# Kernel optimization log

Measured on AMD Instinct MI355X. Metric: run time of the kernel, lower is better.

## Reference

```python
import jax, jax.numpy as jnp
import numpy as np

B, N, F, H = 8, 2048, 64, 1

def setup_inputs() -> dict:
    key = jax.random.key(0)
    k1, k2, k3, k4 = jax.random.split(key, 4)
    return {
        "encode": jax.random.normal(k1, (B, N, F), dtype=jnp.float32),
        "kernel": jax.random.normal(k2, (F, H, F), dtype=jnp.float32) * 0.1,
        "attn_kernel_self": jax.random.normal(k3, (F, H, 1), dtype=jnp.float32) * 0.1,
        "attn_kernel_neighs": jax.random.normal(k4, (F, H, 1), dtype=jnp.float32) * 0.1,
    }

def reference(encode, kernel, attn_kernel_self, attn_kernel_neighs):
    # project: [B,N,F] x [F,H,F] -> [B,N,H,F]
    h = jnp.einsum('bni,iho->bnho', encode, kernel)
    # per-node scalar scores: [B,N,H,1]
    a_self = jnp.einsum('bnhi,iho->bnho', h, attn_kernel_self)
    a_neigh = jnp.einsum('bnhi,iho->bnho', h, attn_kernel_neighs)
    # transpose last three axes (...ABC -> ...CBA): [B,1,H,N]
    a_neigh_t = jnp.transpose(a_neigh, (0, 3, 2, 1))
    # broadcast-sum -> [B,N,H,N] dense logits, leaky_relu(alpha=0.2), softmax over neighbors
    logits = jax.nn.leaky_relu(a_self + a_neigh_t, negative_slope=0.2)
    coef = jax.nn.softmax(logits, axis=-1)
    # mean over heads (axis=2) -> [B,N,N]
    return jnp.mean(coef, axis=2)
```

## Files before the change

kernel.cpp:

```cpp
#include <hip/hip_runtime.h>

#define BB 8
#define NN 2048
#define FF 64
#define LOG2E 1.4426950408889634f

typedef float f32x4 __attribute__((ext_vector_type(4)));

__global__ __launch_bounds__(256) void scores_fused(const float* __restrict__ enc,
                                                    const float* __restrict__ kmat,
                                                    const float* __restrict__ aks,
                                                    const float* __restrict__ akn,
                                                    float* __restrict__ S,
                                                    float* __restrict__ T) {
    __shared__ float ws[FF], wn[FF];
    const int tid = threadIdx.x;
    if (tid < FF) {
        float s = 0.f, t = 0.f;
        #pragma unroll
        for (int o = 0; o < FF; ++o) {
            float k = kmat[tid * FF + o];
            s += k * aks[o];
            t += k * akn[o];
        }
        ws[tid] = s;
        wn[tid] = t;
    }
    __syncthreads();

    const int g = blockIdx.x * 256 + tid;
    const f32x4* e4 = (const f32x4*)(enc + (size_t)g * FF);
    const f32x4* w4 = (const f32x4*)ws;
    const f32x4* v4 = (const f32x4*)wn;
    float s = 0.f, t = 0.f;
    #pragma unroll
    for (int j = 0; j < FF / 4; ++j) {
        f32x4 e = e4[j];
        f32x4 w = w4[j];
        f32x4 v = v4[j];
        s += e.x * w.x + e.y * w.y + e.z * w.z + e.w * w.w;
        t += e.x * v.x + e.y * v.y + e.z * v.z + e.w * v.w;
    }
    S[g] = s * LOG2E;
    T[g] = t * LOG2E;
}

__device__ __forceinline__ float waveMax(float v) {
    #pragma unroll
    for (int o = 32; o > 0; o >>= 1) v = fmaxf(v, __shfl_xor(v, o, 64));
    return v;
}
__device__ __forceinline__ float waveSum(float v) {
    #pragma unroll
    for (int o = 32; o > 0; o >>= 1) v += __shfl_xor(v, o, 64);
    return v;
}
__device__ __forceinline__ float lk(float x) { return fmaxf(x, 0.2f * x); }

#define ROWS_PER_WAVE 4

__global__ __launch_bounds__(256) void softmax_kernel(const float* __restrict__ S,
                                                      const float* __restrict__ T,
                                                      float* __restrict__ out) {
    const int wave = threadIdx.x >> 6;
    const int lane = threadIdx.x & 63;
    const int row0 = (blockIdx.x * 4 + wave) * ROWS_PER_WAVE;
    const int b    = row0 >> 11;

    const f32x4* t4 = (const f32x4*)(T + (size_t)b * NN);

    f32x4 t[8];
    float tm = -3.4e38f;
    #pragma unroll
    for (int j = 0; j < 8; ++j) {
        t[j] = t4[lane + 64 * j];
        tm = fmaxf(tm, fmaxf(fmaxf(t[j].x, t[j].y), fmaxf(t[j].z, t[j].w)));
    }
    const float tmax = waveMax(tm);

    #pragma unroll
    for (int r = 0; r < ROWS_PER_WAVE; ++r) {
        const int row = row0 + r;
        const float s = S[row];
        const float M = lk(s + tmax);

        f32x4 e[8];
        float ls = 0.f;
        #pragma unroll
        for (int j = 0; j < 8; ++j) {
            e[j].x = __builtin_exp2f(lk(s + t[j].x) - M);
            e[j].y = __builtin_exp2f(lk(s + t[j].y) - M);
            e[j].z = __builtin_exp2f(lk(s + t[j].z) - M);
            e[j].w = __builtin_exp2f(lk(s + t[j].w) - M);
            ls += (e[j].x + e[j].y) + (e[j].z + e[j].w);
        }
        ls = waveSum(ls);
        const float inv = 1.f / ls;

        f32x4* o4 = (f32x4*)(out + (size_t)row * NN);
        #pragma unroll
        for (int j = 0; j < 8; ++j) {
            f32x4 o;
            o.x = e[j].x * inv; o.y = e[j].y * inv;
            o.z = e[j].z * inv; o.w = e[j].w * inv;
            __builtin_nontemporal_store(o, &o4[lane + 64 * j]);
        }
    }
}

extern "C" void kernel_launch(void* const* d_in, const int* in_sizes, int n_in,
                              void* d_out, int out_size, void* d_ws, size_t ws_size,
                              hipStream_t stream) {
    const float* enc  = (const float*)d_in[0];
    const float* kmat = (const float*)d_in[1];
    const float* aks  = (const float*)d_in[2];
    const float* akn  = (const float*)d_in[3];
    float* out = (float*)d_out;

    float* W = (float*)d_ws;
    float* S = W;
    float* T = W + BB * NN;

    scores_fused<<<BB * NN / 256, 256, 0, stream>>>(enc, kmat, aks, akn, S, T);
    softmax_kernel<<<BB * NN / (4 * ROWS_PER_WAVE), 256, 0, stream>>>(S, T, out);
}
```

Before: 34.16 us.

## Factor leaky-relu softmax exponentials into per-column tables shared in LDS

Because exp2 is monotonic and leaky_relu(x) = max(x, 0.2x), each output element becomes max(A*E[j], B*F[j]). Here E and F are per-column exponentials of the T scores, computed once per block into shared memory, and A and B are per-row scalars. This replaces the per-element exp2 in the hot loop with two multiplies and a max, and batches the four row-sum reductions. It also swaps the nontemporal stores for plain stores and uses a fast reciprocal. The risks are some precision difference from the factored exponentials and extra LDS traffic, in a kernel that is likely bound by output-write bandwidth anyway.

```diff
diff --git a/kernel.cpp b/kernel.cpp
--- a/kernel.cpp
+++ b/kernel.cpp
@@ -4,8 +4,22 @@
 #define NN 2048
 #define FF 64
 #define LOG2E 1.4426950408889634f
+#define ROWS_PER_BLOCK 16
 
 typedef float f32x4 __attribute__((ext_vector_type(4)));
+
+__device__ __forceinline__ float waveMax(float v) {
+    #pragma unroll
+    for (int o = 32; o > 0; o >>= 1) v = fmaxf(v, __shfl_xor(v, o, 64));
+    return v;
+}
+__device__ __forceinline__ float lk(float x) { return fmaxf(x, 0.2f * x); }
+__device__ __forceinline__ f32x4 vmax4(f32x4 a, f32x4 b) {
+    f32x4 r;
+    r.x = fmaxf(a.x, b.x); r.y = fmaxf(a.y, b.y);
+    r.z = fmaxf(a.z, b.z); r.w = fmaxf(a.w, b.w);
+    return r;
+}
 
 __global__ __launch_bounds__(256) void scores_fused(const float* __restrict__ enc,
                                                     const float* __restrict__ kmat,
@@ -45,65 +59,88 @@
     T[g] = t * LOG2E;
 }
 
-__device__ __forceinline__ float waveMax(float v) {
-    #pragma unroll
-    for (int o = 32; o > 0; o >>= 1) v = fmaxf(v, __shfl_xor(v, o, 64));
-    return v;
-}
-__device__ __forceinline__ float waveSum(float v) {
-    #pragma unroll
-    for (int o = 32; o > 0; o >>= 1) v += __shfl_xor(v, o, 64);
-    return v;
-}
-__device__ __forceinline__ float lk(float x) { return fmaxf(x, 0.2f * x); }
-
-#define ROWS_PER_WAVE 4
-
 __global__ __launch_bounds__(256) void softmax_kernel(const float* __restrict__ S,
                                                       const float* __restrict__ T,
                                                       float* __restrict__ out) {
-    const int wave = threadIdx.x >> 6;
-    const int lane = threadIdx.x & 63;
-    const int row0 = (blockIdx.x * 4 + wave) * ROWS_PER_WAVE;
+    __shared__ float Ez[NN];
+    __shared__ float Fz[NN];
+    __shared__ float wred[4];
+
+    const int tid  = threadIdx.x;
+    const int wave = tid >> 6, lane = tid & 63;
+    const int row0 = blockIdx.x * ROWS_PER_BLOCK;
     const int b    = row0 >> 11;
 
     const f32x4* t4 = (const f32x4*)(T + (size_t)b * NN);
+    f32x4 ta = t4[tid];
+    f32x4 tb = t4[tid + 256];
+    float tm = fmaxf(fmaxf(fmaxf(ta.x, ta.y), fmaxf(ta.z, ta.w)),
+                     fmaxf(fmaxf(tb.x, tb.y), fmaxf(tb.z, tb.w)));
+    tm = waveMax(tm);
+    if (lane == 0) wred[wave] = tm;
+    __syncthreads();
+    const float tmax = fmaxf(fmaxf(wred[0], wred[1]), fmaxf(wred[2], wred[3]));
 
-    f32x4 t[8];
-    float tm = -3.4e38f;
+    f32x4* EL = (f32x4*)Ez;
+    f32x4* FL = (f32x4*)Fz;
+    {
+        f32x4 d, E, F;
+        d.x = ta.x - tmax; d.y = ta.y - tmax; d.z = ta.z - tmax; d.w = ta.w - tmax;
+        E.x = __builtin_exp2f(d.x); E.y = __builtin_exp2f(d.y);
+        E.z = __builtin_exp2f(d.z); E.w = __builtin_exp2f(d.w);
+        F.x = __builtin_exp2f(0.2f * d.x); F.y = __builtin_exp2f(0.2f * d.y);
+        F.z = __builtin_exp2f(0.2f * d.z); F.w = __builtin_exp2f(0.2f * d.w);
+        EL[tid] = E; FL[tid] = F;
+        d.x = tb.x - tmax; d.y = tb.y - tmax; d.z = tb.z - tmax; d.w = tb.w - tmax;
+        E.x = __builtin_exp2f(d.x); E.y = __builtin_exp2f(d.y);
+        E.z = __builtin_exp2f(d.z); E.w = __builtin_exp2f(d.w);
+        F.x = __builtin_exp2f(0.2f * d.x); F.y = __builtin_exp2f(0.2f * d.y);
+        F.z = __builtin_exp2f(0.2f * d.z); F.w = __builtin_exp2f(0.2f * d.w);
+        EL[tid + 256] = E; FL[tid + 256] = F;
+    }
+    __syncthreads();
+
+    const int wrow0 = row0 + wave * 4;
+    float A[4], Bc[4], ls[4];
     #pragma unroll
-    for (int j = 0; j < 8; ++j) {
-        t[j] = t4[lane + 64 * j];
-        tm = fmaxf(tm, fmaxf(fmaxf(t[j].x, t[j].y), fmaxf(t[j].z, t[j].w)));
+    for (int r = 0; r < 4; ++r) {
+        const float s = S[wrow0 + r];
+        const float u = s + tmax;
+        const float M = lk(u);
+        A[r]  = __builtin_exp2f(u - M);
+        Bc[r] = __builtin_exp2f(0.2f * u - M);
+        float l = 0.f;
+        #pragma unroll
+        for (int j = 0; j < 8; ++j) {
+            f32x4 E = EL[lane + 64 * j];
+            f32x4 F = FL[lane + 64 * j];
+            f32x4 e = vmax4(A[r] * E, Bc[r] * F);
+            l += (e.x + e.y) + (e.z + e.w);
+        }
+        ls[r] = l;
     }
-    const float tmax = waveMax(tm);
+    #pragma unroll
+    for (int o = 32; o > 0; o >>= 1) {
+        ls[0] += __shfl_xor(ls[0], o, 64);
+        ls[1] += __shfl_xor(ls[1], o, 64);
+        ls[2] += __shfl_xor(ls[2], o, 64);
+        ls[3] += __shfl_xor(ls[3], o, 64);
+    }
+    #pragma unroll
+    for (int r = 0; r < 4; ++r) {
+        const float inv = __builtin_amdgcn_rcpf(ls[r]);
+        A[r]  *= inv;
+        Bc[r] *= inv;
+    }
 
     #pragma unroll
-    for (int r = 0; r < ROWS_PER_WAVE; ++r) {
-        const int row = row0 + r;
-        const float s = S[row];
-        const float M = lk(s + tmax);
-
-        f32x4 e[8];
-        float ls = 0.f;
+    for (int r = 0; r < 4; ++r) {
+        f32x4* o4 = (f32x4*)(out + (size_t)(wrow0 + r) * NN);
         #pragma unroll
         for (int j = 0; j < 8; ++j) {
-            e[j].x = __builtin_exp2f(lk(s + t[j].x) - M);
-            e[j].y = __builtin_exp2f(lk(s + t[j].y) - M);
-            e[j].z = __builtin_exp2f(lk(s + t[j].z) - M);
-            e[j].w = __builtin_exp2f(lk(s + t[j].w) - M);
-            ls += (e[j].x + e[j].y) + (e[j].z + e[j].w);
-        }
-        ls = waveSum(ls);
-        const float inv = 1.f / ls;
-
-        f32x4* o4 = (f32x4*)(out + (size_t)row * NN);
-        #pragma unroll
-        for (int j = 0; j < 8; ++j) {
-            f32x4 o;
-            o.x = e[j].x * inv; o.y = e[j].y * inv;
-            o.z = e[j].z * inv; o.w = e[j].w * inv;
-            __builtin_nontemporal_store(o, &o4[lane + 64 * j]);
+            f32x4 E = EL[lane + 64 * j];
+            f32x4 F = FL[lane + 64 * j];
+            o4[lane + 64 * j] = vmax4(A[r] * E, Bc[r] * F);
         }
     }
 }
@@ -122,5 +159,5 @@
     float* T = W + BB * NN;
 
     scores_fused<<<BB * NN / 256, 256, 0, stream>>>(enc, kmat, aks, akn, S, T);
-    softmax_kernel<<<BB * NN / (4 * ROWS_PER_WAVE), 256, 0, stream>>>(S, T, out);
+    softmax_kernel<<<BB * NN / ROWS_PER_BLOCK, 256, 0, stream>>>(S, T, out);
 }
```

After: 33.69 us. No clear change (-1.4%).
